# Kernel tuning notes

Hardware: AMD Instinct MI355X
Metric: run time of the kernel (lower is better)

Reference implementation:

```python
import jax, jax.numpy as jnp
import numpy as np

LEAKY_SLOPE = 0.01  # torch nn.LeakyReLU default

def leaky_relu(x):
    return jnp.where(x >= 0, x, LEAKY_SLOPE * x)

def setup_inputs() -> dict:
    key = jax.random.key(0)
    ks = jax.random.split(key, 11)
    B, F, C_IN, H, K, D = 2048, 512, 3, 64, 8, 128  # batch, features, expand, layer_conf[0], bucket_num, bucket_dim
    ASR, MM, OUT = 128, 768, 256
    proj_in = ASR + MM + F * D
    inp = {
        "stat_features": jax.random.uniform(ks[0], (B, F), dtype=jnp.float32),
        "asr_embeddings": jax.random.normal(ks[1], (B, ASR), dtype=jnp.float32),
        "mm_embeddings": jax.random.normal(ks[2], (B, MM), dtype=jnp.float32),
        "linear1_w": jax.random.normal(ks[3], (F, C_IN, H), dtype=jnp.float32) * (1.0 / np.sqrt(C_IN)),
        "linear1_b": jax.random.normal(ks[4], (F, 1, H), dtype=jnp.float32),
        "linear2_w": jax.random.normal(ks[5], (F, H, K), dtype=jnp.float32) * (1.0 / np.sqrt(H)),
        "linear2_b": jax.random.normal(ks[6], (F, 1, K), dtype=jnp.float32),
        "tau": jnp.ones((F, 1, K), dtype=jnp.float32),
        "emb": jax.random.normal(ks[7], (F, K, D), dtype=jnp.float32),
        "proj_w": jax.random.normal(ks[8], (OUT, proj_in), dtype=jnp.float32) * (1.0 / np.sqrt(proj_in)),
        "proj_b": jax.random.normal(ks[9], (OUT,), dtype=jnp.float32) * 0.01,
    }
    return inp

def reference(stat_features, asr_embeddings, mm_embeddings,
              linear1_w, linear1_b, linear2_w, linear2_b, tau, emb,
              proj_w, proj_b):
    # sanitize: NaN -> 0, negatives -> 0
    x = stat_features
    x = jnp.where(jnp.isnan(x) | (x < 0.0), 0.0, x)  # [B, F]

    # auto_dis: per-feature tiny MLP. x is expanded to 3 identical copies -> [B,F,1,3]
    # matmul with [F,3,H] == einsum over the 3 copies.
    B, F = x.shape
    x3 = jnp.broadcast_to(x[:, :, None], (B, F, 3))           # [B,F,3]
    h = jnp.einsum('bfc,fch->bfh', x3, linear1_w) + linear1_b[:, 0, :]  # [B,F,H]
    h = jnp.where(h >= 0, h, LEAKY_SLOPE * h)
    s = jnp.einsum('bfh,fhk->bfk', h, linear2_w) + linear2_b[:, 0, :]   # [B,F,K]
    s = jnp.where(s >= 0, s, LEAKY_SLOPE * s)
    s = s * tau[:, 0, :]
    p = jax.nn.softmax(s, axis=-1)                            # [B,F,K]
    y = jnp.einsum('bfk,fkd->bfd', p, emb)                    # [B,F,D]
    y = y.reshape(B, -1)                                      # [B, F*D] (fc = Identity)

    z = jnp.concatenate([asr_embeddings, mm_embeddings, y], axis=1)
    out = jax.nn.relu(z @ proj_w.T + proj_b)                  # [B, 256]
    return out
```

## Files before the change

### kernel.cpp

```cpp
#include <hip/hip_runtime.h>
#include <hip/hip_bf16.h>
#include <math.h>

#define LEAKY 0.01f
#define B_    2048
#define F_    512
#define H_    64
#define K_    8
#define D_    128
#define ASR_  128
#define MM_   768
#define OUT_  256
#define PROJ_IN 66432
#define ZK    4992
#define NSPLIT 8


typedef unsigned short u16;
typedef u16   u16x8 __attribute__((ext_vector_type(8)));
typedef short s16x8 __attribute__((ext_vector_type(8)));
typedef float f32x4 __attribute__((ext_vector_type(4)));

__device__ __forceinline__ u16 f2bf(float x) {
  unsigned int u = __float_as_uint(x);
  u += 0x7fffu + ((u >> 16) & 1u);
  return (u16)(u >> 16);
}

#define PRODUCER_BLOCKS (512 + 1024 + 896 + 224)

__global__ __launch_bounds__(256) void producer_kernel(
    const float* __restrict__ stat, const float* __restrict__ w1,
    const float* __restrict__ b1v, const float* __restrict__ w2,
    const float* __restrict__ b2v, const float* __restrict__ tauv,
    const float* __restrict__ pw, const float* __restrict__ emb,
    const float* __restrict__ asr, const float* __restrict__ mm,
    u16* __restrict__ A0, u16* __restrict__ Pf, u16* __restrict__ Wn) {
  __shared__ __align__(16) char smem[15616];
  const int bid = blockIdx.x;
  const int t = threadIdx.x;

  if (bid < 512) {
    const int f0 = (bid >> 3) * 8;
    const int o0 = (bid & 7) * 32;
    const int w = t >> 6, lane = t & 63;
    const int fl = lane >> 5, k = (lane >> 2) & 7, dq = lane & 3;
    const int fbase = f0 + 2 * w;
    float4 e[8];
    {
      const float* ep = emb + ((size_t)(fbase + fl) * 8 + k) * 128 + dq * 32;
      #pragma unroll
      for (int j = 0; j < 8; ++j) e[j] = *(const float4*)(ep + j * 4);
    }
    const float* src = pw + (size_t)o0 * PROJ_IN + 896 + (size_t)fbase * 128 + lane * 4;
    const int sl0 = fl * 32 + dq * 8;
    u16* wdst = Wn + (size_t)o0 * ZK + 896 + (size_t)(fbase + fl) * 8 + k;
    float4 vbuf[4];
    #pragma unroll
    for (int i = 0; i < 4; ++i)
      vbuf[i] = *(const float4*)(src + (size_t)i * PROJ_IN);
    #pragma unroll
    for (int r = 0; r < 32; ++r) {
      float4 cur = vbuf[r & 3];
      if (r + 4 < 32)
        vbuf[r & 3] = *(const float4*)(src + (size_t)(r + 4) * PROJ_IN);
      float gp[4] = {0.f, 0.f, 0.f, 0.f};
      #pragma unroll
      for (int j = 0; j < 8; ++j) {
        float px = __shfl(cur.x, sl0 + j);
        float py = __shfl(cur.y, sl0 + j);
        float pz = __shfl(cur.z, sl0 + j);
        float pq = __shfl(cur.w, sl0 + j);
        gp[j & 3] = fmaf(e[j].x, px, gp[j & 3]);
        gp[j & 3] = fmaf(e[j].y, py, gp[j & 3]);
        gp[j & 3] = fmaf(e[j].z, pz, gp[j & 3]);
        gp[j & 3] = fmaf(e[j].w, pq, gp[j & 3]);
      }
      float g = (gp[0] + gp[1]) + (gp[2] + gp[3]);
      g += __shfl_xor(g, 1);
      g += __shfl_xor(g, 2);
      if (dq == 0) wdst[(size_t)r * ZK] = f2bf(g);
    }
  } else if (bid < 1536) {
    const int pb = bid - 512;
    const int f0 = (pb & 127) * 4;
    const int b0 = (pb >> 7) * 256;
    float* s_w1s = (float*)(smem);
    float* s_b1  = (float*)(smem + 1024);
    float* s_w2  = (float*)(smem + 2048);
    float* s_b2  = (float*)(smem + 10240);
    float* s_tau = (float*)(smem + 10368);
    float* s_x   = (float*)(smem + 10496);
    {
      int fl = t >> 6, h = t & 63;
      const float* wf = w1 + (size_t)(f0 + fl) * 192;
      s_w1s[fl * 64 + h] = wf[h] + wf[64 + h] + wf[128 + h];
      s_b1[fl * 64 + h] = b1v[(size_t)(f0 + fl) * 64 + h];
    }
    for (int i = t; i < 4 * 512; i += 256) {
      int fl = i >> 9, idx = i & 511;
      s_w2[fl * 512 + idx] = w2[(size_t)(f0 + fl) * 512 + idx];
    }
    if (t < 32) {
      s_b2[t]  = b2v[f0 * 8 + t];
      s_tau[t] = tauv[f0 * 8 + t];
    }
    {
      float4 sv = *(const float4*)(stat + (size_t)(b0 + t) * F_ + f0);
      float* xr = s_x + t * 5;
      xr[0] = (sv.x >= 0.f) ? sv.x : 0.f;
      xr[1] = (sv.y >= 0.f) ? sv.y : 0.f;
      xr[2] = (sv.z >= 0.f) ? sv.z : 0.f;
      xr[3] = (sv.w >= 0.f) ? sv.w : 0.f;
    }
    __syncthreads();

    const int w = t >> 6;
    const int lane = t & 63;
    const float* w1p = s_w1s + w * 64;
    const float* b1p = s_b1 + w * 64;
    const float* w2p = s_w2 + w * 512;
    float x[4];
    #pragma unroll
    for (int p = 0; p < 4; ++p) x[p] = s_x[(lane + 64 * p) * 5 + w];
    float acc[4][8] = {{0.f}};
    #pragma unroll 4
    for (int i = 0; i < 64; ++i) {
      float wv = w1p[i], bv = b1p[i];
      float4 wa = *(const float4*)(w2p + i * 8);
      float4 wb = *(const float4*)(w2p + i * 8 + 4);
      #pragma unroll
      for (int p = 0; p < 4; ++p) {
        float h0 = fmaf(x[p], wv, bv);
        float h = fmaf(LEAKY, fminf(h0, 0.f), fmaxf(h0, 0.f));
        acc[p][0] = fmaf(h, wa.x, acc[p][0]);
        acc[p][1] = fmaf(h, wa.y, acc[p][1]);
        acc[p][2] = fmaf(h, wa.z, acc[p][2]);
        acc[p][3] = fmaf(h, wa.w, acc[p][3]);
        acc[p][4] = fmaf(h, wb.x, acc[p][4]);
        acc[p][5] = fmaf(h, wb.y, acc[p][5]);
        acc[p][6] = fmaf(h, wb.z, acc[p][6]);
        acc[p][7] = fmaf(h, wb.w, acc[p][7]);
      }
    }
    #pragma unroll
    for (int p = 0; p < 4; ++p) {
      float s[K_];
      float m = -1e30f;
      #pragma unroll
      for (int kk = 0; kk < K_; ++kk) {
        float v = acc[p][kk] + s_b2[w * 8 + kk];
        v = (v >= 0.f) ? v : LEAKY * v;
        v *= s_tau[w * 8 + kk];
        s[kk] = v;
        m = fmaxf(m, v);
      }
      float sum = 0.f;
      #pragma unroll
      for (int kk = 0; kk < K_; ++kk) { s[kk] = __expf(s[kk] - m); sum += s[kk]; }
      float inv = 1.f / sum;
      u16x8 hv;
      #pragma unroll
      for (int kk = 0; kk < K_; ++kk) hv[kk] = f2bf(s[kk] * inv);
      *(u16x8*)(Pf + ((size_t)(f0 + w) * B_ + b0 + lane + 64 * p) * 8) = hv;
    }
  } else if (bid < 2432) {
    const int item = bid - 1536;
    const int cidx = item * 256 + t;
    const int r = cidx / 112, c = cidx % 112;
    float4 v0, v1;
    if (c < 16) {
      const float* s = asr + (size_t)r * ASR_ + c * 8;
      v0 = *(const float4*)(s); v1 = *(const float4*)(s + 4);
    } else {
      const float* s = mm + (size_t)r * MM_ + (c - 16) * 8;
      v0 = *(const float4*)(s); v1 = *(const float4*)(s + 4);
    }
    u16x8 hv = {f2bf(v0.x), f2bf(v0.y), f2bf(v0.z), f2bf(v0.w),
                f2bf(v1.x), f2bf(v1.y), f2bf(v1.z), f2bf(v1.w)};
    *(u16x8*)(A0 + (size_t)r * 896 + c * 8) = hv;
  } else {
    const int item = bid - 2432;
    #pragma unroll
    for (int rr = 0; rr < 4; ++rr) {
      int idx = item * 1024 + rr * 256 + t;
      int o = idx / 896, j = idx % 896;
      Wn[(size_t)o * ZK + j] = f2bf(pw[(size_t)o * PROJ_IN + j]);
    }
  }
}

#define SAS 72
__global__ __launch_bounds__(256) void gemm_kernel(
    const u16* __restrict__ A0, const u16* __restrict__ Pf,
    const u16* __restrict__ Wn, float* __restrict__ part) {
  const int bm0 = blockIdx.x * 64;
  const int bn0 = blockIdx.y * 64;
  const int kz  = blockIdx.z;
  const int it0 = kz * 10;
  const int itn = (kz == 7) ? 8 : 10;
  __shared__ u16 sA[64 * SAS];
  __shared__ u16 sB[64 * SAS];
  const int t = threadIdx.x;
  const int w = t >> 6, L = t & 63;
  const int l16 = L & 15, q8 = (L >> 4) * 8;
  const int wm = (w >> 1) * 32, wn = (w & 1) * 32;
  const int row = t >> 2, lk = t & 3;
  const int pp = t >> 5, pg = t & 31;
  f32x4 acc[2][2] = {{{0.f,0.f,0.f,0.f},{0.f,0.f,0.f,0.f}},
                     {{0.f,0.f,0.f,0.f},{0.f,0.f,0.f,0.f}}};
  u16x8 ra[2], rb[2];

#define LOAD_TILES(IT)                                                        \
  {                                                                           \
    const int k0_ = (IT) * 64;                                                \
    if (k0_ < 896) {                                                          \
      const u16* s_ = A0 + (size_t)(bm0 + row) * 896 + k0_ + lk * 8;          \
      ra[0] = *(const u16x8*)(s_);                                            \
      ra[1] = *(const u16x8*)(s_ + 32);                                       \
    } else {                                                                  \
      const int fb_ = (k0_ - 896) >> 3;                                       \
      const u16* s_ = Pf + ((size_t)(fb_ + pp) * B_ + bm0 + pg) * 8;          \
      ra[0] = *(const u16x8*)(s_);                                            \
      ra[1] = *(const u16x8*)(s_ + 256);                        \
    }                                                                         \
    const u16* sb_ = Wn + (size_t)(bn0 + row) * ZK + k0_ + lk * 8;            \
    rb[0] = *(const u16x8*)(sb_);                                             \
    rb[1] = *(const u16x8*)(sb_ + 32);                                        \
  }

#define STORE_TILES(IT)                                                       \
  {                                                                           \
    if ((IT) * 64 < 896) {                                                    \
      *(u16x8*)&sA[row * SAS + lk * 8]      = ra[0];                          \
      *(u16x8*)&sA[row * SAS + lk * 8 + 32] = ra[1];                          \
    } else {                                                                  \
      *(u16x8*)&sA[pg * SAS + pp * 8]        = ra[0];                         \
      *(u16x8*)&sA[(pg + 32) * SAS + pp * 8] = ra[1];                         \
    }                                                                         \
    *(u16x8*)&sB[row * SAS + lk * 8]      = rb[0];                            \
    *(u16x8*)&sB[row * SAS + lk * 8 + 32] = rb[1];                            \
  }

  LOAD_TILES(it0);
  for (int it = it0; it < it0 + itn; ++it) {
    __syncthreads();
    STORE_TILES(it);
    __syncthreads();
    if (it + 1 < it0 + itn) LOAD_TILES(it + 1);
    #pragma unroll
    for (int ks = 0; ks < 2; ++ks) {
      s16x8 a0 = *(const s16x8*)&sA[(wm + l16) * SAS + ks * 32 + q8];
      s16x8 a1 = *(const s16x8*)&sA[(wm + 16 + l16) * SAS + ks * 32 + q8];
      s16x8 b0 = *(const s16x8*)&sB[(wn + l16) * SAS + ks * 32 + q8];
      s16x8 b1 = *(const s16x8*)&sB[(wn + 16 + l16) * SAS + ks * 32 + q8];
      acc[0][0] = __builtin_amdgcn_mfma_f32_16x16x32_bf16(a0, b0, acc[0][0], 0, 0, 0);
      acc[0][1] = __builtin_amdgcn_mfma_f32_16x16x32_bf16(a0, b1, acc[0][1], 0, 0, 0);
      acc[1][0] = __builtin_amdgcn_mfma_f32_16x16x32_bf16(a1, b0, acc[1][0], 0, 0, 0);
      acc[1][1] = __builtin_amdgcn_mfma_f32_16x16x32_bf16(a1, b1, acc[1][1], 0, 0, 0);
    }
  }
#undef LOAD_TILES
#undef STORE_TILES

  float* dst = part + (size_t)kz * B_ * OUT_;
  #pragma unroll
  for (int mf = 0; mf < 2; ++mf) {
    const int r0 = bm0 + wm + mf * 16 + (L >> 4) * 4;
    #pragma unroll
    for (int nf = 0; nf < 2; ++nf) {
      const int col = bn0 + wn + nf * 16 + l16;
      #pragma unroll
      for (int i = 0; i < 4; ++i)
        dst[(size_t)(r0 + i) * OUT_ + col] = acc[mf][nf][i];
    }
  }
}

__global__ __launch_bounds__(256) void combine_kernel(
    const float* __restrict__ part, const float* __restrict__ pb,
    float* __restrict__ out) {
  const int idx4 = (blockIdx.x * 256 + threadIdx.x) * 4;
  const int o = idx4 & (OUT_ - 1);
  float4 bv = *(const float4*)(pb + o);
  float4 r = bv;
  #pragma unroll
  for (int kz = 0; kz < NSPLIT; ++kz) {
    float4 a = *(const float4*)(part + (size_t)kz * B_ * OUT_ + idx4);
    r.x += a.x; r.y += a.y; r.z += a.z; r.w += a.w;
  }
  r.x = r.x > 0.f ? r.x : 0.f;
  r.y = r.y > 0.f ? r.y : 0.f;
  r.z = r.z > 0.f ? r.z : 0.f;
  r.w = r.w > 0.f ? r.w : 0.f;
  *(float4*)(out + idx4) = r;
}

extern "C" void kernel_launch(void* const* d_in, const int* in_sizes, int n_in,
                              void* d_out, int out_size, void* d_ws, size_t ws_size,
                              hipStream_t stream) {
  (void)in_sizes; (void)n_in; (void)out_size; (void)ws_size;
  const float* stat = (const float*)d_in[0];
  const float* asr  = (const float*)d_in[1];
  const float* mm   = (const float*)d_in[2];
  const float* w1   = (const float*)d_in[3];
  const float* b1   = (const float*)d_in[4];
  const float* w2   = (const float*)d_in[5];
  const float* b2   = (const float*)d_in[6];
  const float* tau  = (const float*)d_in[7];
  const float* emb  = (const float*)d_in[8];
  const float* pw   = (const float*)d_in[9];
  const float* pb   = (const float*)d_in[10];
  float* out = (float*)d_out;
  char* ws = (char*)d_ws;
  u16*   A0   = (u16*)(ws);
  u16*   Pf   = (u16*)(ws + 3670016);
  u16*   Wn   = (u16*)(ws + 20447232);
  float* part = (float*)(ws + 23003136);

  producer_kernel<<<PRODUCER_BLOCKS, 256, 0, stream>>>(
      stat, w1, b1, w2, b2, tau, pw, emb, asr, mm, A0, Pf, Wn);
  gemm_kernel<<<dim3(B_ / 64, OUT_ / 64, NSPLIT), 256, 0, stream>>>(
      A0, Pf, Wn, part);
  combine_kernel<<<B_ * OUT_ / 1024, 256, 0, stream>>>(part, pb, out);
}
```

Measured before the change: 164.5 us.

## Stage proj_w rows through padded LDS double buffer and interleave producer block roles

The proj_w-folding producer branch now loads each proj_w row into a double-buffered, padded shared-memory tile with a three-deep register prefetch, and reads operands from LDS. This replaces the 32 cross-lane shuffles per row. Block indices are also remapped so each group of 83 consecutive blocks mixes all four producer roles, which balances the memory-bound and compute-bound work across the GPU. The cost is a workgroup barrier per row and slightly more shared memory.

```diff
diff --git a/kernel.cpp b/kernel.cpp
--- a/kernel.cpp
+++ b/kernel.cpp
@@ -28,6 +28,8 @@
 }
 
 #define PRODUCER_BLOCKS (512 + 1024 + 896 + 224)
+#define QS 40
+#define FS 164
 
 __global__ __launch_bounds__(256) void producer_kernel(
     const float* __restrict__ stat, const float* __restrict__ w1,
@@ -36,51 +38,60 @@
     const float* __restrict__ pw, const float* __restrict__ emb,
     const float* __restrict__ asr, const float* __restrict__ mm,
     u16* __restrict__ A0, u16* __restrict__ Pf, u16* __restrict__ Wn) {
-  __shared__ __align__(16) char smem[15616];
-  const int bid = blockIdx.x;
+  __shared__ __align__(16) char smem[15872];
   const int t = threadIdx.x;
+  const int grp = blockIdx.x / 83, r83 = blockIdx.x % 83;
+  int bid;
+  if (r83 < 16)      bid = grp * 16 + r83;
+  else if (r83 < 48) bid = 512 + grp * 32 + (r83 - 16);
+  else if (r83 < 76) bid = 1536 + grp * 28 + (r83 - 48);
+  else               bid = 2432 + grp * 7 + (r83 - 76);
 
   if (bid < 512) {
     const int f0 = (bid >> 3) * 8;
     const int o0 = (bid & 7) * 32;
-    const int w = t >> 6, lane = t & 63;
-    const int fl = lane >> 5, k = (lane >> 2) & 7, dq = lane & 3;
-    const int fbase = f0 + 2 * w;
+    float* s_pw = (float*)smem;
+    const int fl = t >> 5, k = (t >> 2) & 7, dq = t & 3;
     float4 e[8];
     {
-      const float* ep = emb + ((size_t)(fbase + fl) * 8 + k) * 128 + dq * 32;
+      const float* ep = emb + ((size_t)(f0 + fl) * 8 + k) * 128 + dq * 32;
       #pragma unroll
       for (int j = 0; j < 8; ++j) e[j] = *(const float4*)(ep + j * 4);
     }
-    const float* src = pw + (size_t)o0 * PROJ_IN + 896 + (size_t)fbase * 128 + lane * 4;
-    const int sl0 = fl * 32 + dq * 8;
-    u16* wdst = Wn + (size_t)o0 * ZK + 896 + (size_t)(fbase + fl) * 8 + k;
-    float4 vbuf[4];
-    #pragma unroll
-    for (int i = 0; i < 4; ++i)
-      vbuf[i] = *(const float4*)(src + (size_t)i * PROJ_IN);
-    #pragma unroll
+    const int cq = (t >> 3) & 3, ci = t & 7;
+    const int wofs = (t >> 5) * FS + cq * QS + ci * 4;
+    const float* pwbase = pw + 896 + (size_t)f0 * 128 + (size_t)o0 * PROJ_IN + t * 4;
+#define LD(R) (*(const float4*)(pwbase + (size_t)(R) * PROJ_IN))
+    float4 nx0 = LD(0), nx1 = LD(1), nx2 = LD(2);
+    *(float4*)(s_pw + wofs) = nx0;
+    nx0 = LD(3);
+    asm volatile("s_waitcnt lgkmcnt(0)" ::: "memory");
+    __builtin_amdgcn_s_barrier();
+    u16* wdst = Wn + (size_t)o0 * ZK + 896 + (size_t)(f0 + fl) * 8 + k;
     for (int r = 0; r < 32; ++r) {
-      float4 cur = vbuf[r & 3];
-      if (r + 4 < 32)
-        vbuf[r & 3] = *(const float4*)(src + (size_t)(r + 4) * PROJ_IN);
-      float gp[4] = {0.f, 0.f, 0.f, 0.f};
+      float* buf  = s_pw + (r & 1) * (8 * FS);
+      float* nbuf = s_pw + ((r + 1) & 1) * (8 * FS);
+      if (r + 1 < 32) *(float4*)(nbuf + wofs) = nx1;
+      nx1 = nx2; nx2 = nx0;
+      if (r + 4 < 32) nx0 = LD(r + 4);
+      const float* pp = buf + fl * FS + dq * QS;
+      float gp0 = 0.f, gp1 = 0.f;
       #pragma unroll
       for (int j = 0; j < 8; ++j) {
-        float px = __shfl(cur.x, sl0 + j);
-        float py = __shfl(cur.y, sl0 + j);
-        float pz = __shfl(cur.z, sl0 + j);
-        float pq = __shfl(cur.w, sl0 + j);
-        gp[j & 3] = fmaf(e[j].x, px, gp[j & 3]);
-        gp[j & 3] = fmaf(e[j].y, py, gp[j & 3]);
-        gp[j & 3] = fmaf(e[j].z, pz, gp[j & 3]);
-        gp[j & 3] = fmaf(e[j].w, pq, gp[j & 3]);
+        float4 p4 = *(const float4*)(pp + j * 4);
+        gp0 = fmaf(e[j].x, p4.x, gp0);
+        gp1 = fmaf(e[j].y, p4.y, gp1);
+        gp0 = fmaf(e[j].z, p4.z, gp0);
+        gp1 = fmaf(e[j].w, p4.w, gp1);
       }
-      float g = (gp[0] + gp[1]) + (gp[2] + gp[3]);
+      float g = gp0 + gp1;
       g += __shfl_xor(g, 1);
       g += __shfl_xor(g, 2);
       if (dq == 0) wdst[(size_t)r * ZK] = f2bf(g);
-    }
+      asm volatile("s_waitcnt lgkmcnt(0)" ::: "memory");
+      __builtin_amdgcn_s_barrier();
+    }
+#undef LD
   } else if (bid < 1536) {
     const int pb = bid - 512;
     const int f0 = (pb & 127) * 4;
```

Result: no change. 167.3 us (+1.7%).
